# Kernel tuning notes

Measured on AMD Instinct MI355X. Metric: run time of the kernel, lower is better.

## Reference

```python
import jax, jax.numpy as jnp
import numpy as np

EMBED_DIM = 512
N_HEADS = 8
HEAD_DIM = EMBED_DIM // N_HEADS
B, S = 4, 2048

def gelu(x):
    # torch F.gelu default = exact erf gelu
    return jax.nn.gelu(x, approximate=False)

def setup_inputs() -> dict:
    key = jax.random.key(0)
    ks = jax.random.split(key, 9)
    sc = 1.0 / np.sqrt(EMBED_DIM)
    inp = {
        'x':   jax.random.normal(ks[0], (B, S, EMBED_DIM), dtype=jnp.float32),
        'Wq':  jax.random.uniform(ks[1], (EMBED_DIM, EMBED_DIM), jnp.float32, -sc, sc),
        'bq':  jax.random.uniform(ks[2], (EMBED_DIM,), jnp.float32, -sc, sc),
        'Wk':  jax.random.uniform(ks[3], (EMBED_DIM, EMBED_DIM), jnp.float32, -sc, sc),
        'bk':  jax.random.uniform(ks[4], (EMBED_DIM,), jnp.float32, -sc, sc),
        'Wv':  jax.random.uniform(ks[5], (EMBED_DIM, EMBED_DIM), jnp.float32, -sc, sc),
        'bv':  jax.random.uniform(ks[6], (EMBED_DIM,), jnp.float32, -sc, sc),
        'Wo':  jax.random.uniform(ks[7], (EMBED_DIM, EMBED_DIM), jnp.float32, -sc, sc),
        'bo':  jax.random.uniform(ks[8], (EMBED_DIM,), jnp.float32, -sc, sc),
    }
    return inp

def reference(x, Wq, bq, Wk, bk, Wv, bv, Wo, bo):
    Bsz, Ssz, _ = x.shape
    def proj(W, b):
        # [B,S,E] -> [B,H,S,D], GELU applied before head split (same math either way)
        h = gelu(jnp.einsum('bse,ef->bsf', x, W.T) + b)
        return h.reshape(Bsz, Ssz, N_HEADS, HEAD_DIM).transpose(0, 2, 1, 3)
    q = proj(Wq, bq)
    k = proj(Wk, bk)
    v = proj(Wv, bv)
    attn = jnp.einsum('bhid,bhjd->bhij', q, k) / np.sqrt(HEAD_DIM).astype(np.float32)
    attn = jax.nn.softmax(attn, axis=-1)
    o = jnp.einsum('bhij,bhjd->bhid', attn, v)
    o = o.transpose(0, 2, 1, 3).reshape(Bsz, Ssz, EMBED_DIM)
    return gelu(jnp.einsum('bse,ef->bsf', o, Wo.T) + bo)
```

## Files before the change

kernel.cpp:

```cpp
#include <hip/hip_runtime.h>
#include <hip/hip_bf16.h>

typedef __bf16 bf16_t;
typedef __bf16 bf16x4 __attribute__((ext_vector_type(4)));
typedef __bf16 bf16x8 __attribute__((ext_vector_type(8)));
typedef float  f32x4  __attribute__((ext_vector_type(4)));
typedef float  f32x8  __attribute__((ext_vector_type(8)));

#define EMBED 512
#define NH    8
#define HD    64
#define SEQ   2048
#define MTOT  8192
#define SCQ   0.18033688011112042f

__device__ __forceinline__ float gelu_f(float x) {
    return 0.5f * x * (1.0f + erff(x * 0.7071067811865475f));
}

__device__ __forceinline__ f32x4 mfma16(bf16x8 a, bf16x8 b, f32x4 c) {
    return __builtin_amdgcn_mfma_f32_16x16x32_bf16(a, b, c, 0, 0, 0);
}

__global__ __launch_bounds__(256)
void convert_kernel(const float* __restrict__ x,  const float* __restrict__ Wq,
                    const float* __restrict__ Wk, const float* __restrict__ Wv,
                    bf16_t* __restrict__ xb, bf16_t* __restrict__ wb)
{
    const int y = blockIdx.y;
    const float* src; bf16_t* dst;
    if (y < 16)      { src = x + (size_t)y * 262144; dst = xb + (size_t)y * 262144; }
    else if (y == 16){ src = Wq; dst = wb; }
    else if (y == 17){ src = Wk; dst = wb + 262144; }
    else             { src = Wv; dst = wb + 524288; }
    const int base = (blockIdx.x * 256 + threadIdx.x) * 16;
    const f32x8 a = *(const f32x8*)(src + base);
    const f32x8 b = *(const f32x8*)(src + base + 8);
    *(bf16x8*)(dst + base)     = __builtin_convertvector(a, bf16x8);
    *(bf16x8*)(dst + base + 8) = __builtin_convertvector(b, bf16x8);
}

template<int MODE, int NTILE>
__global__ __launch_bounds__(256, 3)
void gemm_gelu_kernel(const bf16_t* __restrict__ Xb,
                      const bf16_t* __restrict__ Wb,
                      const float*  __restrict__ Wf,
                      const float*  __restrict__ Bq, const float* __restrict__ Bk,
                      const float*  __restrict__ Bv,
                      bf16_t* __restrict__ O0, bf16_t* __restrict__ O1,
                      bf16_t* __restrict__ O2, float* __restrict__ Of)
{
    constexpr int NTN = NTILE / 32;
    __shared__ __align__(16) bf16_t As[128 * 72];
    __shared__ __align__(16) bf16_t Bs[NTILE * 72];
    const int tid  = threadIdx.x;
    const int lane = tid & 63, w = tid >> 6, quad = lane >> 4, l15 = lane & 15;
    const int m0 = blockIdx.x * 128;
    int mat, n0;
    if (MODE == 0) { mat = blockIdx.y >> 2; n0 = (blockIdx.y & 3) * NTILE; }
    else           { mat = 0;               n0 = blockIdx.y * NTILE; }
    const bf16_t* W  = (MODE == 0) ? (Wb + (size_t)mat * 262144) : nullptr;
    const float*  Bi = (MODE == 1) ? Bq : (mat == 0 ? Bq : (mat == 1 ? Bk : Bv));

    const int wr = (w >> 1) * 64;
    const int wc = (w & 1) * (NTILE / 2);

    const int srow = tid >> 3, scol = (tid & 7) * 8;

    f32x4 acc[4][NTN];
#pragma unroll
    for (int a = 0; a < 4; ++a)
#pragma unroll
        for (int b = 0; b < NTN; ++b) acc[a][b] = f32x4{0.f, 0.f, 0.f, 0.f};

    bf16x8 xp[4];
    bf16x8 wpb[NTN];
    f32x8  wpf[NTN];

#pragma unroll
    for (int it = 0; it < 4; ++it)
        xp[it] = *(const bf16x8*)(Xb + (size_t)(m0 + it * 32 + srow) * EMBED + scol);
#pragma unroll
    for (int it = 0; it < NTN; ++it) {
        const int r = it * 32 + srow;
        if (MODE == 0) wpb[it] = *(const bf16x8*)(W + (size_t)(n0 + r) * EMBED + scol);
        else           wpf[it] = *(const f32x8*)(Wf + (size_t)(n0 + r) * EMBED + scol);
    }

#pragma unroll 1
    for (int kt = 0; kt < 8; ++kt) {
        __syncthreads();
#pragma unroll
        for (int it = 0; it < 4; ++it)
            *(bf16x8*)(As + (it * 32 + srow) * 72 + scol) = xp[it];
#pragma unroll
        for (int it = 0; it < NTN; ++it) {
            const int r = it * 32 + srow;
            if (MODE == 0) *(bf16x8*)(Bs + r * 72 + scol) = wpb[it];
            else *(bf16x8*)(Bs + r * 72 + scol) = __builtin_convertvector(wpf[it], bf16x8);
        }
        if (kt < 7) {
            const int k1 = (kt + 1) * 64;
#pragma unroll
            for (int it = 0; it < 4; ++it)
                xp[it] = *(const bf16x8*)(Xb + (size_t)(m0 + it * 32 + srow) * EMBED + k1 + scol);
#pragma unroll
            for (int it = 0; it < NTN; ++it) {
                const int r = it * 32 + srow;
                if (MODE == 0) wpb[it] = *(const bf16x8*)(W + (size_t)(n0 + r) * EMBED + k1 + scol);
                else           wpf[it] = *(const f32x8*)(Wf + (size_t)(n0 + r) * EMBED + k1 + scol);
            }
        }
        __syncthreads();
#pragma unroll
        for (int ks = 0; ks < 2; ++ks) {
            const int ko = (ks * 4 + quad) * 8;
            bf16x8 av[4], bv[NTN];
#pragma unroll
            for (int mt = 0; mt < 4; ++mt)
                av[mt] = *(const bf16x8*)(As + (wr + mt * 16 + l15) * 72 + ko);
#pragma unroll
            for (int nt = 0; nt < NTN; ++nt)
                bv[nt] = *(const bf16x8*)(Bs + (wc + nt * 16 + l15) * 72 + ko);
#pragma unroll
            for (int mt = 0; mt < 4; ++mt)
#pragma unroll
                for (int nt = 0; nt < NTN; ++nt)
                    acc[mt][nt] = mfma16(av[mt], bv[nt], acc[mt][nt]);
        }
    }

    float biasv[NTN];
#pragma unroll
    for (int nt = 0; nt < NTN; ++nt)
        biasv[nt] = Bi[n0 + wc + nt * 16 + l15];
#pragma unroll
    for (int mt = 0; mt < 4; ++mt) {
        const int mb = m0 + wr + mt * 16 + quad * 4;
        const int bb = mb >> 11, s0 = mb & (SEQ - 1);
#pragma unroll
        for (int nt = 0; nt < NTN; ++nt) {
            const int fc = n0 + wc + nt * 16 + l15;
            const int h = fc >> 6, d = fc & 63;
            float vv[4];
#pragma unroll
            for (int i = 0; i < 4; ++i) vv[i] = gelu_f(acc[mt][nt][i] + biasv[nt]);
            if (MODE == 1) {
#pragma unroll
                for (int i = 0; i < 4; ++i) Of[(size_t)(mb + i) * EMBED + fc] = vv[i];
            } else if (mat == 0) {
#pragma unroll
                for (int i = 0; i < 4; ++i)
                    O0[(((size_t)(bb * NH + h)) * SEQ + s0 + i) * HD + d] = (bf16_t)(vv[i] * SCQ);
            } else if (mat == 1) {
#pragma unroll
                for (int i = 0; i < 4; ++i)
                    O1[(((size_t)(bb * NH + h)) * SEQ + s0 + i) * HD + d] = (bf16_t)vv[i];
            } else {
                bf16x4 pk;
#pragma unroll
                for (int i = 0; i < 4; ++i) pk[i] = (bf16_t)vv[i];
                *(bf16x4*)(O2 + ((size_t)(bb * NH + h) * HD + d) * SEQ + s0) = pk;
            }
        }
    }
}

__global__ __launch_bounds__(256, 3)
void flash_attn_kernel(const bf16_t* __restrict__ Q,
                       const bf16_t* __restrict__ K,
                       const bf16_t* __restrict__ Vt,
                       bf16_t* __restrict__ Og)
{
    __shared__ __align__(16) bf16_t Ks[2][64 * 72];
    __shared__ __align__(16) bf16_t Vs[2][64 * 72];
    __shared__ __align__(16) bf16_t Ps[4][16 * 72];

    const int tid  = threadIdx.x;
    const int lane = tid & 63, w = tid >> 6, quad = lane >> 4, l15 = lane & 15;
    const int bh = blockIdx.y;
    const int q0 = blockIdx.x * 64;
    const size_t baseQK = (size_t)bh * SEQ * HD;
    const size_t baseV  = (size_t)bh * HD * SEQ;
    const int wm = w * 16;

    bf16x8 qf[2];
#pragma unroll
    for (int ks = 0; ks < 2; ++ks)
        qf[ks] = *(const bf16x8*)(Q + baseQK + (size_t)(q0 + wm + l15) * HD + ks * 32 + quad * 8);

    float lsum = 0.f;
    f32x4 oacc[4];
#pragma unroll
    for (int nt = 0; nt < 4; ++nt) oacc[nt] = f32x4{0.f, 0.f, 0.f, 0.f};

    bf16_t* Pw = Ps[w];
    const int r0 = tid >> 3, c0 = (tid & 7) * 8;
    bf16x8 kr0, kr1, vr0, vr1;

    kr0 = *(const bf16x8*)(K + baseQK + (size_t)r0 * HD + c0);
    kr1 = *(const bf16x8*)(K + baseQK + (size_t)(r0 + 32) * HD + c0);
    vr0 = *(const bf16x8*)(Vt + baseV + (size_t)r0 * SEQ + c0);
    vr1 = *(const bf16x8*)(Vt + baseV + (size_t)(r0 + 32) * SEQ + c0);
    *(bf16x8*)(Ks[0] + r0 * 72 + c0)        = kr0;
    *(bf16x8*)(Ks[0] + (r0 + 32) * 72 + c0) = kr1;
    *(bf16x8*)(Vs[0] + r0 * 72 + c0)        = vr0;
    *(bf16x8*)(Vs[0] + (r0 + 32) * 72 + c0) = vr1;
    kr0 = *(const bf16x8*)(K + baseQK + (size_t)(64 + r0) * HD + c0);
    kr1 = *(const bf16x8*)(K + baseQK + (size_t)(64 + r0 + 32) * HD + c0);
    vr0 = *(const bf16x8*)(Vt + baseV + (size_t)r0 * SEQ + 64 + c0);
    vr1 = *(const bf16x8*)(Vt + baseV + (size_t)(r0 + 32) * SEQ + 64 + c0);

#pragma unroll 1
    for (int t = 0; t < 32; ++t) {
        __syncthreads();
        if (t + 1 < 32) {
            bf16_t* Kn = Ks[(t + 1) & 1];
            bf16_t* Vn = Vs[(t + 1) & 1];
            *(bf16x8*)(Kn + r0 * 72 + c0)        = kr0;
            *(bf16x8*)(Kn + (r0 + 32) * 72 + c0) = kr1;
            *(bf16x8*)(Vn + r0 * 72 + c0)        = vr0;
            *(bf16x8*)(Vn + (r0 + 32) * 72 + c0) = vr1;
        }
        if (t + 2 < 32) {
            const int kv = (t + 2) * 64;
            kr0 = *(const bf16x8*)(K + baseQK + (size_t)(kv + r0) * HD + c0);
            kr1 = *(const bf16x8*)(K + baseQK + (size_t)(kv + r0 + 32) * HD + c0);
            vr0 = *(const bf16x8*)(Vt + baseV + (size_t)r0 * SEQ + kv + c0);
            vr1 = *(const bf16x8*)(Vt + baseV + (size_t)(r0 + 32) * SEQ + kv + c0);
        }

        const bf16_t* Kb = Ks[t & 1];
        const bf16_t* Vb = Vs[t & 1];

        f32x4 sf[4];
#pragma unroll
        for (int jt = 0; jt < 4; ++jt) sf[jt] = f32x4{0.f, 0.f, 0.f, 0.f};
#pragma unroll
        for (int ks = 0; ks < 2; ++ks) {
            const int ko = ks * 32 + quad * 8;
#pragma unroll
            for (int jt = 0; jt < 4; ++jt) {
                const bf16x8 a = *(const bf16x8*)(Kb + (jt * 16 + l15) * 72 + ko);
                sf[jt] = mfma16(a, qf[ks], sf[jt]);
            }
        }

#pragma unroll
        for (int jt = 0; jt < 4; ++jt) {
#pragma unroll
            for (int i = 0; i < 4; ++i) {
                const float pv = exp2f(sf[jt][i] - 8.f);
                sf[jt][i] = pv;
                lsum += pv;
            }
            const bf16x4 pk = __builtin_convertvector(sf[jt], bf16x4);
            *(bf16x4*)(Pw + l15 * 72 + jt * 16 + quad * 4) = pk;
        }

#pragma unroll
        for (int c = 0; c < 2; ++c) {
            const int ko = c * 32 + quad * 8;
            const bf16x8 a = *(const bf16x8*)(Pw + l15 * 72 + ko);
#pragma unroll
            for (int nt = 0; nt < 4; ++nt) {
                const bf16x8 b = *(const bf16x8*)(Vb + (nt * 16 + l15) * 72 + ko);
                oacc[nt] = mfma16(a, b, oacc[nt]);
            }
        }
    }

    float rs = lsum;
    rs += __shfl_xor(rs, 16);
    rs += __shfl_xor(rs, 32);
    const int bidx = bh >> 3, h = bh & 7;
    float lf[4];
#pragma unroll
    for (int i = 0; i < 4; ++i)
        lf[i] = __shfl(rs, (lane & 48) | (quad * 4 + i));
#pragma unroll
    for (int nt = 0; nt < 4; ++nt)
#pragma unroll
        for (int i = 0; i < 4; ++i) {
            const int s = q0 + wm + quad * 4 + i;
            const int d = nt * 16 + l15;
            Og[((size_t)(bidx * SEQ + s)) * EMBED + h * HD + d] =
                (bf16_t)(oacc[nt][i] / lf[i]);
        }
}

extern "C" void kernel_launch(void* const* d_in, const int* in_sizes, int n_in,
                              void* d_out, int out_size, void* d_ws, size_t ws_size,
                              hipStream_t stream)
{
    const float* x  = (const float*)d_in[0];
    const float* Wq = (const float*)d_in[1];
    const float* bq = (const float*)d_in[2];
    const float* Wk = (const float*)d_in[3];
    const float* bk = (const float*)d_in[4];
    const float* Wv = (const float*)d_in[5];
    const float* bv = (const float*)d_in[6];
    const float* Wo = (const float*)d_in[7];
    const float* bo = (const float*)d_in[8];
    float* out = (float*)d_out;

    const size_t NE = (size_t)MTOT * EMBED;
    bf16_t* xb  = (bf16_t*)d_out;
    bf16_t* Qw  = (bf16_t*)d_out + NE;
    bf16_t* Kw  = (bf16_t*)d_ws;
    bf16_t* Vtw = Kw + NE;
    bf16_t* Ow  = Vtw + NE;
    bf16_t* Wb  = Ow;

    convert_kernel<<<dim3(64, 19), 256, 0, stream>>>(x, Wq, Wk, Wv, xb, Wb);
    gemm_gelu_kernel<0, 128><<<dim3(64, 12), 256, 0, stream>>>(
        xb, Wb, nullptr, bq, bk, bv, Qw, Kw, Vtw, nullptr);
    flash_attn_kernel<<<dim3(32, 32), 256, 0, stream>>>(Qw, Kw, Vtw, Ow);
    gemm_gelu_kernel<1, 64><<<dim3(64, 8), 256, 0, stream>>>(
        Ow, nullptr, Wo, bo, nullptr, nullptr, nullptr, nullptr, nullptr, out);
}
```

Before: 191.5 us.

## Swizzle flash-attention LDS tiles, raise occupancy, add MFMA priority hints

Replaces the padded 72-stride shared-memory tiles for K, V and P with unpadded 64-stride tiles that use an XOR swizzle of the column offset. This avoids bank conflicts while shrinking shared memory per block. The launch-bounds minimum is raised from 3 to 4 blocks per SM, which adds register pressure. The row-sum is kept as a vector accumulator, and s_setprio raises wave priority around the MFMA sections to help interleave them with other waves.

```diff
diff --git a/kernel.cpp b/kernel.cpp
--- a/kernel.cpp
+++ b/kernel.cpp
@@ -166,15 +166,15 @@
     }
 }
 
-__global__ __launch_bounds__(256, 3)
+__global__ __launch_bounds__(256, 4)
 void flash_attn_kernel(const bf16_t* __restrict__ Q,
                        const bf16_t* __restrict__ K,
                        const bf16_t* __restrict__ Vt,
                        bf16_t* __restrict__ Og)
 {
-    __shared__ __align__(16) bf16_t Ks[2][64 * 72];
-    __shared__ __align__(16) bf16_t Vs[2][64 * 72];
-    __shared__ __align__(16) bf16_t Ps[4][16 * 72];
+    __shared__ __align__(16) bf16_t Ks[2][64 * 64];
+    __shared__ __align__(16) bf16_t Vs[2][64 * 64];
+    __shared__ __align__(16) bf16_t Ps[4][16 * 64];
 
     const int tid  = threadIdx.x;
     const int lane = tid & 63, w = tid >> 6, quad = lane >> 4, l15 = lane & 15;
@@ -183,29 +183,31 @@
     const size_t baseQK = (size_t)bh * SEQ * HD;
     const size_t baseV  = (size_t)bh * HD * SEQ;
     const int wm = w * 16;
+    const int cx = (l15 & 7) << 3;
 
     bf16x8 qf[2];
 #pragma unroll
     for (int ks = 0; ks < 2; ++ks)
         qf[ks] = *(const bf16x8*)(Q + baseQK + (size_t)(q0 + wm + l15) * HD + ks * 32 + quad * 8);
 
-    float lsum = 0.f;
+    f32x4 lacc = f32x4{0.f, 0.f, 0.f, 0.f};
     f32x4 oacc[4];
 #pragma unroll
     for (int nt = 0; nt < 4; ++nt) oacc[nt] = f32x4{0.f, 0.f, 0.f, 0.f};
 
     bf16_t* Pw = Ps[w];
     const int r0 = tid >> 3, c0 = (tid & 7) * 8;
+    const int sA = (r0 << 6) + (c0 ^ ((r0 & 7) << 3));
     bf16x8 kr0, kr1, vr0, vr1;
 
     kr0 = *(const bf16x8*)(K + baseQK + (size_t)r0 * HD + c0);
     kr1 = *(const bf16x8*)(K + baseQK + (size_t)(r0 + 32) * HD + c0);
     vr0 = *(const bf16x8*)(Vt + baseV + (size_t)r0 * SEQ + c0);
     vr1 = *(const bf16x8*)(Vt + baseV + (size_t)(r0 + 32) * SEQ + c0);
-    *(bf16x8*)(Ks[0] + r0 * 72 + c0)        = kr0;
-    *(bf16x8*)(Ks[0] + (r0 + 32) * 72 + c0) = kr1;
-    *(bf16x8*)(Vs[0] + r0 * 72 + c0)        = vr0;
-    *(bf16x8*)(Vs[0] + (r0 + 32) * 72 + c0) = vr1;
+    *(bf16x8*)(Ks[0] + sA)        = kr0;
+    *(bf16x8*)(Ks[0] + sA + 2048) = kr1;
+    *(bf16x8*)(Vs[0] + sA)        = vr0;
+    *(bf16x8*)(Vs[0] + sA + 2048) = vr1;
     kr0 = *(const bf16x8*)(K + baseQK + (size_t)(64 + r0) * HD + c0);
     kr1 = *(const bf16x8*)(K + baseQK + (size_t)(64 + r0 + 32) * HD + c0);
     vr0 = *(const bf16x8*)(Vt + baseV + (size_t)r0 * SEQ + 64 + c0);
@@ -217,10 +219,10 @@
         if (t + 1 < 32) {
             bf16_t* Kn = Ks[(t + 1) & 1];
             bf16_t* Vn = Vs[(t + 1) & 1];
-            *(bf16x8*)(Kn + r0 * 72 + c0)        = kr0;
-            *(bf16x8*)(Kn + (r0 + 32) * 72 + c0) = kr1;
-            *(bf16x8*)(Vn + r0 * 72 + c0)        = vr0;
-            *(bf16x8*)(Vn + (r0 + 32) * 72 + c0) = vr1;
+            *(bf16x8*)(Kn + sA)        = kr0;
+            *(bf16x8*)(Kn + sA + 2048) = kr1;
+            *(bf16x8*)(Vn + sA)        = vr0;
+            *(bf16x8*)(Vn + sA + 2048) = vr1;
         }
         if (t + 2 < 32) {
             const int kv = (t + 2) * 64;
@@ -236,41 +238,42 @@
         f32x4 sf[4];
 #pragma unroll
         for (int jt = 0; jt < 4; ++jt) sf[jt] = f32x4{0.f, 0.f, 0.f, 0.f};
+        __builtin_amdgcn_s_setprio(1);
 #pragma unroll
         for (int ks = 0; ks < 2; ++ks) {
-            const int ko = ks * 32 + quad * 8;
+            const int ko = (ks * 32 + quad * 8) ^ cx;
 #pragma unroll
             for (int jt = 0; jt < 4; ++jt) {
-                const bf16x8 a = *(const bf16x8*)(Kb + (jt * 16 + l15) * 72 + ko);
+                const bf16x8 a = *(const bf16x8*)(Kb + ((jt * 16 + l15) << 6) + ko);
                 sf[jt] = mfma16(a, qf[ks], sf[jt]);
             }
         }
+        __builtin_amdgcn_s_setprio(0);
 
 #pragma unroll
         for (int jt = 0; jt < 4; ++jt) {
 #pragma unroll
-            for (int i = 0; i < 4; ++i) {
-                const float pv = exp2f(sf[jt][i] - 8.f);
-                sf[jt][i] = pv;
-                lsum += pv;
-            }
+            for (int i = 0; i < 4; ++i) sf[jt][i] = exp2f(sf[jt][i] - 8.f);
+            lacc += sf[jt];
             const bf16x4 pk = __builtin_convertvector(sf[jt], bf16x4);
-            *(bf16x4*)(Pw + l15 * 72 + jt * 16 + quad * 4) = pk;
-        }
-
+            *(bf16x4*)(Pw + (l15 << 6) + ((jt * 16 + quad * 4) ^ cx)) = pk;
+        }
+
+        __builtin_amdgcn_s_setprio(1);
 #pragma unroll
         for (int c = 0; c < 2; ++c) {
-            const int ko = c * 32 + quad * 8;
-            const bf16x8 a = *(const bf16x8*)(Pw + l15 * 72 + ko);
+            const int ko = (c * 32 + quad * 8) ^ cx;
+            const bf16x8 a = *(const bf16x8*)(Pw + (l15 << 6) + ko);
 #pragma unroll
             for (int nt = 0; nt < 4; ++nt) {
-                const bf16x8 b = *(const bf16x8*)(Vb + (nt * 16 + l15) * 72 + ko);
+                const bf16x8 b = *(const bf16x8*)(Vb + ((nt * 16 + l15) << 6) + ko);
                 oacc[nt] = mfma16(a, b, oacc[nt]);
             }
         }
+        __builtin_amdgcn_s_setprio(0);
     }
 
-    float rs = lsum;
+    float rs = (lacc[0] + lacc[1]) + (lacc[2] + lacc[3]);
     rs += __shfl_xor(rs, 16);
     rs += __shfl_xor(rs, 32);
     const int bidx = bh >> 3, h = bh & 7;
```

Measured after the change: 186.2 us. -2.8%, faster.
